# Optimization experiments

Measured on AMD Instinct MI355X. Metric: run time of the kernel, lower is better.

The kernel has to match this reference:

```python
import jax, jax.numpy as jnp
import numpy as np

V_IN, V_OUT = 128, 128
E_IN, E_OUT = 64, 64
H, L, D = 256, 2, 2
DEC_H = D * L * H  # 1024
S_IN, B, S_OUT = 128, 512, 64


def _lstm_step(h, c, x, W_ih, W_hh, b):
    # PyTorch gate order: i, f, g, o
    gates = x @ W_ih.T + h @ W_hh.T + b
    i, f, g, o = jnp.split(gates, 4, axis=-1)
    c = jax.nn.sigmoid(f) * c + jax.nn.sigmoid(i) * jnp.tanh(g)
    h = jax.nn.sigmoid(o) * jnp.tanh(c)
    return h, c


def _run_lstm_dir(x_seq, W_ih, W_hh, b, reverse):
    # x_seq: [S, B, in]; returns hidden sequence [S, B, H], final (h, c)
    Bsz = x_seq.shape[1]
    Hd = W_hh.shape[1]
    init = (jnp.zeros((Bsz, Hd), x_seq.dtype), jnp.zeros((Bsz, Hd), x_seq.dtype))

    def step(carry, x):
        h, c = _lstm_step(carry[0], carry[1], x, W_ih, W_hh, b)
        return (h, c), h

    (hf, cf), hs = jax.lax.scan(step, init, x_seq, reverse=reverse)
    return hs, hf, cf


def setup_inputs() -> dict:
    key = jax.random.key(0)
    ks = jax.random.split(key, 20)
    s = 0.05
    inp = {}
    inp["input_tokens"] = jax.random.randint(ks[0], (S_IN, B), 0, V_IN, dtype=jnp.int32)
    inp["output_tokens"] = jax.random.randint(ks[1], (B, S_OUT), 0, V_OUT, dtype=jnp.int32)
    inp["in_emb"] = jax.random.normal(ks[2], (V_IN, E_IN), jnp.float32) * s
    # encoder layer 0: input E_IN; layer 1: input D*H. Leading dim 2 = directions.
    inp["enc_W_ih0"] = jax.random.normal(ks[3], (2, 4 * H, E_IN), jnp.float32) * s
    inp["enc_W_hh0"] = jax.random.normal(ks[4], (2, 4 * H, H), jnp.float32) * s
    inp["enc_b0"] = jax.random.normal(ks[5], (2, 4 * H), jnp.float32) * s
    inp["enc_W_ih1"] = jax.random.normal(ks[6], (2, 4 * H, D * H), jnp.float32) * s
    inp["enc_W_hh1"] = jax.random.normal(ks[7], (2, 4 * H, H), jnp.float32) * s
    inp["enc_b1"] = jax.random.normal(ks[8], (2, 4 * H), jnp.float32) * s
    inp["out_emb"] = jax.random.normal(ks[9], (V_OUT, E_OUT), jnp.float32) * s
    inp["dec_W_ih"] = jax.random.normal(ks[10], (4 * DEC_H, E_OUT), jnp.float32) * s
    inp["dec_W_hh"] = jax.random.normal(ks[11], (4 * DEC_H, DEC_H), jnp.float32) * s
    inp["dec_b"] = jax.random.normal(ks[12], (4 * DEC_H,), jnp.float32) * s
    inp["proj_W"] = jax.random.normal(ks[13], (V_OUT, DEC_H), jnp.float32) * s
    inp["proj_b"] = jax.random.normal(ks[14], (V_OUT,), jnp.float32) * s
    return inp


def reference(input_tokens, output_tokens, in_emb,
              enc_W_ih0, enc_W_hh0, enc_b0,
              enc_W_ih1, enc_W_hh1, enc_b1,
              out_emb, dec_W_ih, dec_W_hh, dec_b, proj_W, proj_b):
    # ---- encoder: 2-layer bidirectional LSTM over [S_in, B] ----
    x = in_emb[input_tokens]  # [S, B, E_IN]
    h_list, c_list = [], []
    for W_ih, W_hh, b in ((enc_W_ih0, enc_W_hh0, enc_b0),
                          (enc_W_ih1, enc_W_hh1, enc_b1)):
        hs_f, hf, cf = _run_lstm_dir(x, W_ih[0], W_hh[0], b[0], False)
        hs_b, hb, cb = _run_lstm_dir(x, W_ih[1], W_hh[1], b[1], True)
        x = jnp.concatenate([hs_f, hs_b], axis=-1)  # [S, B, 2H]
        h_list += [hf, hb]
        c_list += [cf, cb]
    Bsz = x.shape[1]
    # PyTorch h_n order: (l0_fwd, l0_bwd, l1_fwd, l1_bwd) -> swapaxes+reshape
    h0 = jnp.stack(h_list, axis=1).reshape(Bsz, -1)  # [B, D*L*H]
    c0 = jnp.stack(c_list, axis=1).reshape(Bsz, -1)

    # ---- decoder: teacher-forced LSTMCell loop ----
    tok_in = output_tokens[:, :-1].T   # [T-1, B]
    tok_next = output_tokens[:, 1:].T  # [T-1, B]

    def step(carry, toks):
        h, c = carry
        t_in, t_next = toks
        e = out_emb[t_in]                                 # [B, E_OUT]
        h, c = _lstm_step(h, c, e, dec_W_ih, dec_W_hh, dec_b)
        logits = c @ proj_W.T + proj_b                    # NOTE: proj on CELL, as in source
        greedy = jnp.argmax(logits, axis=1)
        lp = jax.nn.log_softmax(logits, axis=-1)
        logp = jnp.take_along_axis(lp, t_next[:, None], axis=1)[:, 0]
        return (h, c), (greedy, logp)

    _, (decoded_tokens, log_probs) = jax.lax.scan(step, (h0, c0), (tok_in, tok_next))
    cum_log_probs = jnp.sum(log_probs, axis=0)  # [B]
    return decoded_tokens, cum_log_probs
```

## Files before the change

kernel.cpp:

```cpp
#include <hip/hip_runtime.h>
#include <math.h>

#define B 512
#define S_IN 128
#define S_OUT 64
#define T_DEC 63

#define O_H0   0
#define O_H1   (512*1024)
#define O_C    (2*512*1024)
#define O_CUM  (3*512*1024)
#define O_HS0  (O_CUM + 512)
#define O_P1   (O_HS0 + 128*512*512)

template<int MODE>
__global__ __launch_bounds__(256)
void enc_step(const float* __restrict__ Wih, const float* __restrict__ Whh,
              const float* __restrict__ bias, const int* __restrict__ tok,
              const float* __restrict__ emb, const float* __restrict__ seqin,
              const float* __restrict__ h_in, float* __restrict__ h_out,
              float* __restrict__ c_st, float* __restrict__ seqout,
              const float* __restrict__ p1, int t)
{
    constexpr int KE = (MODE==0) ? 64 : (MODE==2 ? 512 : 0);
    constexpr int K  = KE + 256;
    constexpr int NK = K/16;

    const int dir   = blockIdx.z;
    const int t_eff = dir ? (S_IN-1-t) : t;
    const int hseg  = (MODE==0) ? dir*256 : 512 + dir*256;

    const float* Wih_d = Wih + (size_t)dir*1024*KE;
    const float* Whh_d = Whh + (size_t)dir*1024*256;
    const float* b_d   = bias + dir*1024;

    __shared__ float As[16][64];
    __shared__ float Bs[16][64];

    const int tid = threadIdx.x;
    const int bm0 = blockIdx.x*64;
    const int bn0 = blockIdx.y*64;

    const int la_m  = tid >> 2;
    const int la_k  = (tid & 3) << 2;
    const int a_row = bm0 + la_m;

    const int lb_n = tid >> 2;
    const int lb_k = (tid & 3) << 2;
    const int n_g  = bn0 + lb_n;
    const int b_j  = (n_g & 3)*256 + (n_g >> 2);

    int tokidx = 0;
    if (MODE==0) tokidx = tok[t_eff*B + a_row];

    const int tm = (tid >> 4) << 2;
    const int tn = (tid & 15) << 2;

    float acc[4][4] = {};

    auto loadA = [&](int kt) -> float4 {
        int k = kt*16 + la_k;
        if (MODE==0) {
            if (k < 64) return *(const float4*)&emb[(size_t)tokidx*64 + k];
            return *(const float4*)&h_in[(size_t)a_row*1024 + hseg + (k-64)];
        } else if (MODE==2) {
            if (k < 512) return *(const float4*)&seqin[((size_t)t_eff*B + a_row)*512 + k];
            return *(const float4*)&h_in[(size_t)a_row*1024 + hseg + (k-512)];
        } else {
            return *(const float4*)&h_in[(size_t)a_row*1024 + hseg + k];
        }
    };
    auto loadB = [&](int kt) -> float4 {
        int k = kt*16 + lb_k;
        if (KE && k < KE) return *(const float4*)&Wih_d[(size_t)b_j*KE + k];
        return *(const float4*)&Whh_d[(size_t)b_j*256 + (k-KE)];
    };

    float4 aR = loadA(0), bR = loadB(0);
    for (int kt=0; kt<NK; ++kt) {
        __syncthreads();
        As[la_k+0][la_m]=aR.x; As[la_k+1][la_m]=aR.y; As[la_k+2][la_m]=aR.z; As[la_k+3][la_m]=aR.w;
        Bs[lb_k+0][lb_n]=bR.x; Bs[lb_k+1][lb_n]=bR.y; Bs[lb_k+2][lb_n]=bR.z; Bs[lb_k+3][lb_n]=bR.w;
        __syncthreads();
        if (kt+1 < NK) { aR = loadA(kt+1); bR = loadB(kt+1); }
        #pragma unroll
        for (int k=0;k<16;k++){
            const float4 a = *(const float4*)&As[k][tm];
            const float4 b = *(const float4*)&Bs[k][tn];
            acc[0][0]+=a.x*b.x; acc[0][1]+=a.x*b.y; acc[0][2]+=a.x*b.z; acc[0][3]+=a.x*b.w;
            acc[1][0]+=a.y*b.x; acc[1][1]+=a.y*b.y; acc[1][2]+=a.y*b.z; acc[1][3]+=a.y*b.w;
            acc[2][0]+=a.z*b.x; acc[2][1]+=a.z*b.y; acc[2][2]+=a.z*b.z; acc[2][3]+=a.z*b.w;
            acc[3][0]+=a.w*b.x; acc[3][1]+=a.w*b.y; acc[3][2]+=a.w*b.z; acc[3][3]+=a.w*b.w;
        }
    }

    const int jh = (bn0 + tn) >> 2;
    const float bi = b_d[0*256 + jh];
    const float bf = b_d[1*256 + jh];
    const float bg = b_d[2*256 + jh];
    const float bo = b_d[3*256 + jh];
    #pragma unroll
    for (int i=0;i<4;i++){
        const int brow = bm0 + tm + i;
        float xi = acc[i][0] + bi;
        float xf = acc[i][1] + bf;
        float xg = acc[i][2] + bg;
        float xo = acc[i][3] + bo;
        if (MODE==1) {
            const float4 pv = *(const float4*)&p1[((size_t)dir*512 + brow)*1024 + bn0 + tn];
            xi += pv.x; xf += pv.y; xg += pv.z; xo += pv.w;
        }
        float ig = 1.f/(1.f+expf(-xi));
        float fg = 1.f/(1.f+expf(-xf));
        float gg = tanhf(xg);
        float og = 1.f/(1.f+expf(-xo));
        size_t ci = (size_t)brow*1024 + hseg + jh;
        float cn = fg*c_st[ci] + ig*gg;
        float hn = og*tanhf(cn);
        c_st[ci]  = cn;
        h_out[ci] = hn;
        if (MODE==0) seqout[((size_t)t_eff*B + brow)*512 + dir*256 + jh] = hn;
    }
}

template<int MODE>
__global__ __launch_bounds__(128)
void gemm128(const float* __restrict__ Wih, const float* __restrict__ Whh,
             const float* __restrict__ bias, const int* __restrict__ tok,
             const float* __restrict__ emb, const float* __restrict__ hs0,
             const float* __restrict__ h_in, float* __restrict__ h_out,
             float* __restrict__ c_st, float* __restrict__ p1out, int t_or_s0)
{
    constexpr int KE = (MODE==0) ? 64 : 0;
    constexpr int K  = (MODE==0) ? 1088 : 512;
    constexpr int NK = K/16;
    constexpr int HH = (MODE==0) ? 1024 : 256;

    const int dir = (MODE==1) ? blockIdx.z : 0;

    __shared__ float As[16][64];
    __shared__ float Bs[16][64];

    const int tid = threadIdx.x;
    const int bm0 = blockIdx.x*64;
    const int bn0 = blockIdx.y*64;

    const int la_m  = tid >> 1;
    const int la_k  = (tid & 1) << 3;
    const int a_row = bm0 + la_m;

    const int srel  = (MODE==1) ? (blockIdx.x >> 3) : 0;
    const int sabs  = (MODE==1) ? (t_or_s0 + srel) : 0;
    const int t_eff = (MODE==1) ? (dir ? (S_IN-1-sabs) : sabs) : 0;
    const int a_b   = a_row & 511;

    const int n_g = bn0 + la_m;
    const int b_j = (n_g & 3)*HH + (n_g >> 2);

    const float* Wih_d = (MODE==1) ? (Wih + (size_t)dir*1024*512) : Wih;

    int tokidx = 0;
    if (MODE==0) tokidx = tok[a_row*S_OUT + t_or_s0];

    const int tm = (tid >> 3) << 2;
    const int tn = (tid & 7) << 3;

    float acc[4][8] = {};

    auto loadA = [&](int kt, int q) -> float4 {
        int k = kt*16 + la_k + q*4;
        if (MODE==0) {
            if (k < 64) return *(const float4*)&emb[(size_t)tokidx*64 + k];
            return *(const float4*)&h_in[(size_t)a_row*1024 + (k-64)];
        }
        return *(const float4*)&hs0[((size_t)t_eff*B + a_b)*512 + k];
    };
    auto loadB = [&](int kt, int q) -> float4 {
        int k = kt*16 + la_k + q*4;
        if (MODE==0) {
            if (k < 64) return *(const float4*)&Wih[(size_t)b_j*64 + k];
            return *(const float4*)&Whh[(size_t)b_j*1024 + (k-64)];
        }
        return *(const float4*)&Wih_d[(size_t)b_j*512 + k];
    };

    float4 aR0 = loadA(0,0), aR1 = loadA(0,1);
    float4 bR0 = loadB(0,0), bR1 = loadB(0,1);
    for (int kt=0; kt<NK; ++kt) {
        __syncthreads();
        As[la_k+0][la_m]=aR0.x; As[la_k+1][la_m]=aR0.y; As[la_k+2][la_m]=aR0.z; As[la_k+3][la_m]=aR0.w;
        As[la_k+4][la_m]=aR1.x; As[la_k+5][la_m]=aR1.y; As[la_k+6][la_m]=aR1.z; As[la_k+7][la_m]=aR1.w;
        Bs[la_k+0][la_m]=bR0.x; Bs[la_k+1][la_m]=bR0.y; Bs[la_k+2][la_m]=bR0.z; Bs[la_k+3][la_m]=bR0.w;
        Bs[la_k+4][la_m]=bR1.x; Bs[la_k+5][la_m]=bR1.y; Bs[la_k+6][la_m]=bR1.z; Bs[la_k+7][la_m]=bR1.w;
        __syncthreads();
        if (kt+1 < NK) {
            aR0 = loadA(kt+1,0); aR1 = loadA(kt+1,1);
            bR0 = loadB(kt+1,0); bR1 = loadB(kt+1,1);
        }
        #pragma unroll
        for (int k=0;k<16;k++){
            const float4 a  = *(const float4*)&As[k][tm];
            const float4 b0 = *(const float4*)&Bs[k][tn];
            const float4 b1 = *(const float4*)&Bs[k][tn+4];
            acc[0][0]+=a.x*b0.x; acc[0][1]+=a.x*b0.y; acc[0][2]+=a.x*b0.z; acc[0][3]+=a.x*b0.w;
            acc[0][4]+=a.x*b1.x; acc[0][5]+=a.x*b1.y; acc[0][6]+=a.x*b1.z; acc[0][7]+=a.x*b1.w;
            acc[1][0]+=a.y*b0.x; acc[1][1]+=a.y*b0.y; acc[1][2]+=a.y*b0.z; acc[1][3]+=a.y*b0.w;
            acc[1][4]+=a.y*b1.x; acc[1][5]+=a.y*b1.y; acc[1][6]+=a.y*b1.z; acc[1][7]+=a.y*b1.w;
            acc[2][0]+=a.z*b0.x; acc[2][1]+=a.z*b0.y; acc[2][2]+=a.z*b0.z; acc[2][3]+=a.z*b0.w;
            acc[2][4]+=a.z*b1.x; acc[2][5]+=a.z*b1.y; acc[2][6]+=a.z*b1.z; acc[2][7]+=a.z*b1.w;
            acc[3][0]+=a.w*b0.x; acc[3][1]+=a.w*b0.y; acc[3][2]+=a.w*b0.z; acc[3][3]+=a.w*b0.w;
            acc[3][4]+=a.w*b1.x; acc[3][5]+=a.w*b1.y; acc[3][6]+=a.w*b1.z; acc[3][7]+=a.w*b1.w;
        }
    }

    if (MODE==0) {
        const int jh0 = (bn0 + tn) >> 2;
        #pragma unroll
        for (int u=0;u<2;u++){
            const int jh = jh0 + u;
            const float bi = bias[0*1024 + jh];
            const float bf = bias[1*1024 + jh];
            const float bg = bias[2*1024 + jh];
            const float bo = bias[3*1024 + jh];
            #pragma unroll
            for (int i=0;i<4;i++){
                const int brow = bm0 + tm + i;
                float xi = acc[i][4*u+0] + bi;
                float xf = acc[i][4*u+1] + bf;
                float xg = acc[i][4*u+2] + bg;
                float xo = acc[i][4*u+3] + bo;
                float ig = 1.f/(1.f+expf(-xi));
                float fg = 1.f/(1.f+expf(-xf));
                float gg = tanhf(xg);
                float og = 1.f/(1.f+expf(-xo));
                size_t ci = (size_t)brow*1024 + jh;
                float cn = fg*c_st[ci] + ig*gg;
                float hn = og*tanhf(cn);
                c_st[ci]  = cn;
                h_out[ci] = hn;
            }
        }
    } else {
        #pragma unroll
        for (int i=0;i<4;i++){
            const int r = bm0 + tm + i;
            size_t base = ((size_t)(srel*2 + dir)*512 + (r & 511))*1024 + bn0 + tn;
            *(float4*)&p1out[base]   = *(float4*)&acc[i][0];
            *(float4*)&p1out[base+4] = *(float4*)&acc[i][4];
        }
    }
}

__global__ __launch_bounds__(256)
void proj2(const float* __restrict__ c, const float* __restrict__ pW,
           const float* __restrict__ pb, const int* __restrict__ out_tok,
           float* __restrict__ cum, float* __restrict__ dout, int t)
{
    __shared__ float cs[8][1024];
    __shared__ float ls[8][128];
    const int tid = threadIdx.x;
    const int b0 = blockIdx.x*8;
    #pragma unroll
    for (int r=0;r<8;r++)
        *(float4*)&cs[r][tid*4] = *(const float4*)&c[(size_t)(b0+r)*1024 + tid*4];
    __syncthreads();

    const int wave = tid >> 6, lane = tid & 63;
    const int col  = wave*32 + (lane & 31);
    const int rb   = (lane >> 5) * 4;
    float a0=0.f,a1=0.f,a2=0.f,a3=0.f;
    for (int k=0;k<1024;k+=4){
        const float4 w = *(const float4*)&pW[(size_t)col*1024 + k];
        const float4 c0 = *(const float4*)&cs[rb+0][k];
        const float4 c1 = *(const float4*)&cs[rb+1][k];
        const float4 c2 = *(const float4*)&cs[rb+2][k];
        const float4 c3 = *(const float4*)&cs[rb+3][k];
        a0 += w.x*c0.x + w.y*c0.y + w.z*c0.z + w.w*c0.w;
        a1 += w.x*c1.x + w.y*c1.y + w.z*c1.z + w.w*c1.w;
        a2 += w.x*c2.x + w.y*c2.y + w.z*c2.z + w.w*c2.w;
        a3 += w.x*c3.x + w.y*c3.y + w.z*c3.z + w.w*c3.w;
    }
    const float bb = pb[col];
    ls[rb+0][col]=a0+bb; ls[rb+1][col]=a1+bb; ls[rb+2][col]=a2+bb; ls[rb+3][col]=a3+bb;
    __syncthreads();

    #pragma unroll
    for (int rr=0;rr<2;rr++){
        const int r = wave*2 + rr, b = b0 + r;
        float v0 = ls[r][lane], v1 = ls[r][lane+64];
        float mv; int mi;
        if (v1 > v0) { mv = v1; mi = lane+64; } else { mv = v0; mi = lane; }
        #pragma unroll
        for (int o=32;o>=1;o>>=1){
            float ov = __shfl_xor(mv, o);
            int   oi = __shfl_xor(mi, o);
            if (ov > mv || (ov == mv && oi < mi)) { mv = ov; mi = oi; }
        }
        float e = expf(v0 - mv) + expf(v1 - mv);
        #pragma unroll
        for (int o=32;o>=1;o>>=1) e += __shfl_xor(e, o);
        if (lane == 0){
            const int tnx = out_tok[b*S_OUT + t + 1];
            const float lv = ls[r][tnx];
            const float logp = lv - mv - logf(e);
            const float cn = ((t==0) ? 0.f : cum[b]) + logp;
            cum[b] = cn;
            dout[T_DEC*B + b] = cn;
            dout[t*B + b] = (float)mi;
        }
    }
}

__global__ void zero_kernel(float* __restrict__ p, int n4){
    int i = blockIdx.x*blockDim.x + threadIdx.x;
    if (i < n4) *(float4*)&p[i*4] = float4{0.f,0.f,0.f,0.f};
}

extern "C" void kernel_launch(void* const* d_in, const int* in_sizes, int n_in,
                              void* d_out, int out_size, void* d_ws, size_t ws_size,
                              hipStream_t stream)
{
    const int*   input_tokens  = (const int*)d_in[0];
    const int*   output_tokens = (const int*)d_in[1];
    const float* in_emb  = (const float*)d_in[2];
    const float* eWih0   = (const float*)d_in[3];
    const float* eWhh0   = (const float*)d_in[4];
    const float* eb0     = (const float*)d_in[5];
    const float* eWih1   = (const float*)d_in[6];
    const float* eWhh1   = (const float*)d_in[7];
    const float* eb1     = (const float*)d_in[8];
    const float* out_emb = (const float*)d_in[9];
    const float* dWih    = (const float*)d_in[10];
    const float* dWhh    = (const float*)d_in[11];
    const float* db      = (const float*)d_in[12];
    const float* pW      = (const float*)d_in[13];
    const float* pb      = (const float*)d_in[14];

    size_t ws_fl = ws_size / 4;
    if (ws_fl < (size_t)O_P1) return;

    int CH = 0;
    if      (ws_fl >= (size_t)O_P1 + 16u*1048576u) CH = 16;
    else if (ws_fl >= (size_t)O_P1 +  8u*1048576u) CH = 8;
    else if (ws_fl >= (size_t)O_P1 +  4u*1048576u) CH = 4;
    else if (ws_fl >= (size_t)O_P1 +  2u*1048576u) CH = 2;

    float* ws  = (float*)d_ws;
    float* out = (float*)d_out;

    float* h[2] = { ws + O_H0, ws + O_H1 };
    float* c    = ws + O_C;
    float* cum  = ws + O_CUM;
    float* hs0  = ws + O_HS0;
    float* p1   = ws + O_P1;

    zero_kernel<<<(O_HS0/4 + 255)/256, 256, 0, stream>>>(ws, O_HS0/4);

    for (int t=0;t<S_IN;t++)
        enc_step<0><<<dim3(8,16,2),256,0,stream>>>(eWih0, eWhh0, eb0,
            input_tokens, in_emb, nullptr, h[t&1], h[(t+1)&1], c, hs0, nullptr, t);

    if (CH) {
        for (int s0=0; s0<S_IN; s0+=CH) {
            gemm128<1><<<dim3(CH*8,16,2),128,0,stream>>>(eWih1, nullptr, nullptr,
                nullptr, nullptr, hs0, nullptr, nullptr, nullptr, p1, s0);
            for (int s=s0; s<s0+CH; ++s)
                enc_step<1><<<dim3(8,16,2),256,0,stream>>>(eWih1, eWhh1, eb1,
                    nullptr, nullptr, nullptr, h[s&1], h[(s+1)&1], c, nullptr,
                    p1 + (size_t)(s-s0)*2*512*1024, s);
        }
    } else {
        for (int t=0;t<S_IN;t++)
            enc_step<2><<<dim3(8,16,2),256,0,stream>>>(eWih1, eWhh1, eb1,
                nullptr, nullptr, hs0, h[t&1], h[(t+1)&1], c, nullptr, nullptr, t);
    }

    for (int t=0;t<T_DEC;t++){
        gemm128<0><<<dim3(8,64,1),128,0,stream>>>(dWih, dWhh, db,
            output_tokens, out_emb, nullptr, h[t&1], h[(t+1)&1], c, nullptr, t);
        proj2<<<64,256,0,stream>>>(c, pW, pb, output_tokens, cum, out, t);
    }
}
```

Before: 16.89 ms.

## Fuse decoder loop into a single persistent kernel with grid barriers

Replaces the 63 per-step decoder launches (gate GEMM plus separate projection/softmax kernel) with one persistent 512-block kernel that loops over time steps. A software grid barrier built on an atomic counter separates the gate update from the projection, and the projection from the next step. This removes about 126 kernel launches and their gaps. In exchange, all 512 blocks must be resident at once to avoid deadlock, and the projection now handles one batch row per block, re-reading proj_W from global memory for every row.

```diff
diff --git a/kernel.cpp b/kernel.cpp
--- a/kernel.cpp
+++ b/kernel.cpp
@@ -7,11 +7,11 @@
 #define T_DEC 63
 
 #define O_H0   0
-#define O_H1   (512*1024)
-#define O_C    (2*512*1024)
-#define O_CUM  (3*512*1024)
-#define O_HS0  (O_CUM + 512)
-#define O_P1   (O_HS0 + 128*512*512)
+#define O_H1   524288
+#define O_C    1048576
+#define O_BAR  1572864
+#define O_HS0  1572868
+#define O_P1   (O_HS0 + 33554432)
 
 template<int MODE>
 __global__ __launch_bounds__(256)
@@ -123,20 +123,12 @@
     }
 }
 
-template<int MODE>
 __global__ __launch_bounds__(128)
-void gemm128(const float* __restrict__ Wih, const float* __restrict__ Whh,
-             const float* __restrict__ bias, const int* __restrict__ tok,
-             const float* __restrict__ emb, const float* __restrict__ hs0,
-             const float* __restrict__ h_in, float* __restrict__ h_out,
-             float* __restrict__ c_st, float* __restrict__ p1out, int t_or_s0)
+void gemm_p1(const float* __restrict__ Wih, const float* __restrict__ hs0,
+             float* __restrict__ p1out, int s0)
 {
-    constexpr int KE = (MODE==0) ? 64 : 0;
-    constexpr int K  = (MODE==0) ? 1088 : 512;
-    constexpr int NK = K/16;
-    constexpr int HH = (MODE==0) ? 1024 : 256;
-
-    const int dir = (MODE==1) ? blockIdx.z : 0;
+    constexpr int NK = 512/16;
+    const int dir = blockIdx.z;
 
     __shared__ float As[16][64];
     __shared__ float Bs[16][64];
@@ -149,18 +141,15 @@
     const int la_k  = (tid & 1) << 3;
     const int a_row = bm0 + la_m;
 
-    const int srel  = (MODE==1) ? (blockIdx.x >> 3) : 0;
-    const int sabs  = (MODE==1) ? (t_or_s0 + srel) : 0;
-    const int t_eff = (MODE==1) ? (dir ? (S_IN-1-sabs) : sabs) : 0;
+    const int srel  = blockIdx.x >> 3;
+    const int sabs  = s0 + srel;
+    const int t_eff = dir ? (S_IN-1-sabs) : sabs;
     const int a_b   = a_row & 511;
 
     const int n_g = bn0 + la_m;
-    const int b_j = (n_g & 3)*HH + (n_g >> 2);
-
-    const float* Wih_d = (MODE==1) ? (Wih + (size_t)dir*1024*512) : Wih;
-
-    int tokidx = 0;
-    if (MODE==0) tokidx = tok[a_row*S_OUT + t_or_s0];
+    const int b_j = (n_g & 3)*256 + (n_g >> 2);
+
+    const float* Wih_d = Wih + (size_t)dir*1024*512;
 
     const int tm = (tid >> 3) << 2;
     const int tn = (tid & 7) << 3;
@@ -169,18 +158,10 @@
 
     auto loadA = [&](int kt, int q) -> float4 {
         int k = kt*16 + la_k + q*4;
-        if (MODE==0) {
-            if (k < 64) return *(const float4*)&emb[(size_t)tokidx*64 + k];
-            return *(const float4*)&h_in[(size_t)a_row*1024 + (k-64)];
-        }
         return *(const float4*)&hs0[((size_t)t_eff*B + a_b)*512 + k];
     };
     auto loadB = [&](int kt, int q) -> float4 {
         int k = kt*16 + la_k + q*4;
-        if (MODE==0) {
-            if (k < 64) return *(const float4*)&Wih[(size_t)b_j*64 + k];
-            return *(const float4*)&Whh[(size_t)b_j*1024 + (k-64)];
-        }
         return *(const float4*)&Wih_d[(size_t)b_j*512 + k];
     };
 
@@ -213,8 +194,101 @@
         }
     }
 
-    if (MODE==0) {
-        const int jh0 = (bn0 + tn) >> 2;
+    #pragma unroll
+    for (int i=0;i<4;i++){
+        const int r = bm0 + tm + i;
+        size_t base = ((size_t)(srel*2 + dir)*512 + (r & 511))*1024 + bn0 + tn;
+        *(float4*)&p1out[base]   = *(float4*)&acc[i][0];
+        *(float4*)&p1out[base+4] = *(float4*)&acc[i][4];
+    }
+}
+
+__device__ __forceinline__ void grid_bar(unsigned* cnt, unsigned target)
+{
+    __syncthreads();
+    if (threadIdx.x == 0) {
+        __threadfence();
+        atomicAdd(cnt, 1u);
+        while (__hip_atomic_load(cnt, __ATOMIC_ACQUIRE, __HIP_MEMORY_SCOPE_AGENT) < target) {
+            __builtin_amdgcn_s_sleep(2);
+        }
+        __threadfence();
+    }
+    __syncthreads();
+}
+
+__global__ __launch_bounds__(128)
+void dec_persist(const float* __restrict__ Wih, const float* __restrict__ Whh,
+                 const float* __restrict__ bias, const int* __restrict__ tok,
+                 const float* __restrict__ emb, const float* __restrict__ pW,
+                 const float* __restrict__ pb, float* __restrict__ h0b,
+                 float* __restrict__ h1b, float* __restrict__ c_st,
+                 unsigned* __restrict__ bar, float* __restrict__ dout)
+{
+    __shared__ float As[16][64];
+    __shared__ float Bs[16][64];
+    __shared__ float cs[1024];
+    __shared__ float ls[128];
+
+    const int b   = blockIdx.x, tid = threadIdx.x;
+    const int bm0 = (b & 7) << 6;
+    const int bn0 = (b >> 3) << 6;
+
+    const int la_m  = tid >> 1;
+    const int la_k  = (tid & 1) << 3;
+    const int a_row = bm0 + la_m;
+    const int n_g   = bn0 + la_m;
+    const int b_j   = (n_g & 3)*1024 + (n_g >> 2);
+    const int tm    = (tid >> 3) << 2;
+    const int tn    = (tid & 7) << 3;
+    const int jh0   = (bn0 + tn) >> 2;
+
+    for (int t = 0; t < T_DEC; ++t) {
+        const float* h_in  = (t & 1) ? h1b : h0b;
+        float*       h_out = (t & 1) ? h0b : h1b;
+        const int tokidx = tok[a_row*S_OUT + t];
+
+        float acc[4][8] = {};
+        auto loadA = [&](int kt, int q) -> float4 {
+            int k = kt*16 + la_k + q*4;
+            if (k < 64) return *(const float4*)&emb[(size_t)tokidx*64 + k];
+            return *(const float4*)&h_in[(size_t)a_row*1024 + (k-64)];
+        };
+        auto loadB = [&](int kt, int q) -> float4 {
+            int k = kt*16 + la_k + q*4;
+            if (k < 64) return *(const float4*)&Wih[(size_t)b_j*64 + k];
+            return *(const float4*)&Whh[(size_t)b_j*1024 + (k-64)];
+        };
+
+        float4 aR0 = loadA(0,0), aR1 = loadA(0,1);
+        float4 bR0 = loadB(0,0), bR1 = loadB(0,1);
+        for (int kt=0; kt<68; ++kt) {
+            __syncthreads();
+            As[la_k+0][la_m]=aR0.x; As[la_k+1][la_m]=aR0.y; As[la_k+2][la_m]=aR0.z; As[la_k+3][la_m]=aR0.w;
+            As[la_k+4][la_m]=aR1.x; As[la_k+5][la_m]=aR1.y; As[la_k+6][la_m]=aR1.z; As[la_k+7][la_m]=aR1.w;
+            Bs[la_k+0][la_m]=bR0.x; Bs[la_k+1][la_m]=bR0.y; Bs[la_k+2][la_m]=bR0.z; Bs[la_k+3][la_m]=bR0.w;
+            Bs[la_k+4][la_m]=bR1.x; Bs[la_k+5][la_m]=bR1.y; Bs[la_k+6][la_m]=bR1.z; Bs[la_k+7][la_m]=bR1.w;
+            __syncthreads();
+            if (kt+1 < 68) {
+                aR0 = loadA(kt+1,0); aR1 = loadA(kt+1,1);
+                bR0 = loadB(kt+1,0); bR1 = loadB(kt+1,1);
+            }
+            #pragma unroll
+            for (int k=0;k<16;k++){
+                const float4 a  = *(const float4*)&As[k][tm];
+                const float4 b0 = *(const float4*)&Bs[k][tn];
+                const float4 b1 = *(const float4*)&Bs[k][tn+4];
+                acc[0][0]+=a.x*b0.x; acc[0][1]+=a.x*b0.y; acc[0][2]+=a.x*b0.z; acc[0][3]+=a.x*b0.w;
+                acc[0][4]+=a.x*b1.x; acc[0][5]+=a.x*b1.y; acc[0][6]+=a.x*b1.z; acc[0][7]+=a.x*b1.w;
+                acc[1][0]+=a.y*b0.x; acc[1][1]+=a.y*b0.y; acc[1][2]+=a.y*b0.z; acc[1][3]+=a.y*b0.w;
+                acc[1][4]+=a.y*b1.x; acc[1][5]+=a.y*b1.y; acc[1][6]+=a.y*b1.z; acc[1][7]+=a.y*b1.w;
+                acc[2][0]+=a.z*b0.x; acc[2][1]+=a.z*b0.y; acc[2][2]+=a.z*b0.z; acc[2][3]+=a.z*b0.w;
+                acc[2][4]+=a.z*b1.x; acc[2][5]+=a.z*b1.y; acc[2][6]+=a.z*b1.z; acc[2][7]+=a.z*b1.w;
+                acc[3][0]+=a.w*b0.x; acc[3][1]+=a.w*b0.y; acc[3][2]+=a.w*b0.z; acc[3][3]+=a.w*b0.w;
+                acc[3][4]+=a.w*b1.x; acc[3][5]+=a.w*b1.y; acc[3][6]+=a.w*b1.z; acc[3][7]+=a.w*b1.w;
+            }
+        }
+
         #pragma unroll
         for (int u=0;u<2;u++){
             const int jh = jh0 + u;
@@ -240,74 +314,47 @@
                 h_out[ci] = hn;
             }
         }
-    } else {
+
+        grid_bar(bar, (unsigned)(2*t+1) * 512u);
+
         #pragma unroll
-        for (int i=0;i<4;i++){
-            const int r = bm0 + tm + i;
-            size_t base = ((size_t)(srel*2 + dir)*512 + (r & 511))*1024 + bn0 + tn;
-            *(float4*)&p1out[base]   = *(float4*)&acc[i][0];
-            *(float4*)&p1out[base+4] = *(float4*)&acc[i][4];
-        }
-    }
-}
-
-__global__ __launch_bounds__(256)
-void proj2(const float* __restrict__ c, const float* __restrict__ pW,
-           const float* __restrict__ pb, const int* __restrict__ out_tok,
-           float* __restrict__ cum, float* __restrict__ dout, int t)
-{
-    __shared__ float cs[8][1024];
-    __shared__ float ls[8][128];
-    const int tid = threadIdx.x;
-    const int b0 = blockIdx.x*8;
-    #pragma unroll
-    for (int r=0;r<8;r++)
-        *(float4*)&cs[r][tid*4] = *(const float4*)&c[(size_t)(b0+r)*1024 + tid*4];
-    __syncthreads();
-
-    const int wave = tid >> 6, lane = tid & 63;
-    const int col  = wave*32 + (lane & 31);
-    const int rb   = (lane >> 5) * 4;
-    float a0=0.f,a1=0.f,a2=0.f,a3=0.f;
-    for (int k=0;k<1024;k+=4){
-        const float4 w = *(const float4*)&pW[(size_t)col*1024 + k];
-        const float4 c0 = *(const float4*)&cs[rb+0][k];
-        const float4 c1 = *(const float4*)&cs[rb+1][k];
-        const float4 c2 = *(const float4*)&cs[rb+2][k];
-        const float4 c3 = *(const float4*)&cs[rb+3][k];
-        a0 += w.x*c0.x + w.y*c0.y + w.z*c0.z + w.w*c0.w;
-        a1 += w.x*c1.x + w.y*c1.y + w.z*c1.z + w.w*c1.w;
-        a2 += w.x*c2.x + w.y*c2.y + w.z*c2.z + w.w*c2.w;
-        a3 += w.x*c3.x + w.y*c3.y + w.z*c3.z + w.w*c3.w;
-    }
-    const float bb = pb[col];
-    ls[rb+0][col]=a0+bb; ls[rb+1][col]=a1+bb; ls[rb+2][col]=a2+bb; ls[rb+3][col]=a3+bb;
-    __syncthreads();
-
-    #pragma unroll
-    for (int rr=0;rr<2;rr++){
-        const int r = wave*2 + rr, b = b0 + r;
-        float v0 = ls[r][lane], v1 = ls[r][lane+64];
-        float mv; int mi;
-        if (v1 > v0) { mv = v1; mi = lane+64; } else { mv = v0; mi = lane; }
-        #pragma unroll
-        for (int o=32;o>=1;o>>=1){
-            float ov = __shfl_xor(mv, o);
-            int   oi = __shfl_xor(mi, o);
-            if (ov > mv || (ov == mv && oi < mi)) { mv = ov; mi = oi; }
-        }
-        float e = expf(v0 - mv) + expf(v1 - mv);
-        #pragma unroll
-        for (int o=32;o>=1;o>>=1) e += __shfl_xor(e, o);
-        if (lane == 0){
-            const int tnx = out_tok[b*S_OUT + t + 1];
-            const float lv = ls[r][tnx];
-            const float logp = lv - mv - logf(e);
-            const float cn = ((t==0) ? 0.f : cum[b]) + logp;
-            cum[b] = cn;
-            dout[T_DEC*B + b] = cn;
-            dout[t*B + b] = (float)mi;
-        }
+        for (int q=0;q<2;q++)
+            *(float4*)&cs[(q*128+tid)*4] = *(const float4*)&c_st[(size_t)b*1024 + (q*128+tid)*4];
+        __syncthreads();
+        {
+            float a0 = 0.f;
+            for (int k=0;k<1024;k+=4){
+                const float4 w  = *(const float4*)&pW[(size_t)tid*1024 + k];
+                const float4 c0 = *(const float4*)&cs[k];
+                a0 += w.x*c0.x + w.y*c0.y + w.z*c0.z + w.w*c0.w;
+            }
+            ls[tid] = a0 + pb[tid];
+        }
+        __syncthreads();
+        if (tid < 64) {
+            const int lane = tid;
+            const float v0 = ls[lane], v1 = ls[lane+64];
+            float mv; int mi;
+            if (v1 > v0){ mv=v1; mi=lane+64; } else { mv=v0; mi=lane; }
+            #pragma unroll
+            for (int o=32;o>=1;o>>=1){
+                const float ov = __shfl_xor(mv, o);
+                const int   oi = __shfl_xor(mi, o);
+                if (ov > mv || (ov == mv && oi < mi)){ mv=ov; mi=oi; }
+            }
+            float e = expf(v0-mv) + expf(v1-mv);
+            #pragma unroll
+            for (int o=32;o>=1;o>>=1) e += __shfl_xor(e, o);
+            if (lane == 0){
+                const int tnx = tok[b*S_OUT + t + 1];
+                const float logp = ls[tnx] - mv - logf(e);
+                const float cn = ((t==0)?0.f:dout[T_DEC*B + b]) + logp;
+                dout[T_DEC*B + b] = cn;
+                dout[t*B + b] = (float)mi;
+            }
+        }
+
+        grid_bar(bar, (unsigned)(2*t+2) * 512u);
     }
 }
 
@@ -345,14 +392,14 @@
     else if (ws_fl >= (size_t)O_P1 +  4u*1048576u) CH = 4;
     else if (ws_fl >= (size_t)O_P1 +  2u*1048576u) CH = 2;
 
-    float* ws  = (float*)d_ws;
-    float* out = (float*)d_out;
-
-    float* h[2] = { ws + O_H0, ws + O_H1 };
-    float* c    = ws + O_C;
-    float* cum  = ws + O_CUM;
-    float* hs0  = ws + O_HS0;
-    float* p1   = ws + O_P1;
+    float* ws   = (float*)d_ws;
+    float* dout = (float*)d_out;
+
+    float* h[2]   = { ws + O_H0, ws + O_H1 };
+    float* c      = ws + O_C;
+    unsigned* bar = (unsigned*)(ws + O_BAR);
+    float* hs0    = ws + O_HS0;
+    float* p1     = ws + O_P1;
 
     zero_kernel<<<(O_HS0/4 + 255)/256, 256, 0, stream>>>(ws, O_HS0/4);
 
@@ -362,8 +409,7 @@
 
     if (CH) {
         for (int s0=0; s0<S_IN; s0+=CH) {
-            gemm128<1><<<dim3(CH*8,16,2),128,0,stream>>>(eWih1, nullptr, nullptr,
-                nullptr, nullptr, hs0, nullptr, nullptr, nullptr, p1, s0);
+            gemm_p1<<<dim3(CH*8,16,2),128,0,stream>>>(eWih1, hs0, p1, s0);
             for (int s=s0; s<s0+CH; ++s)
                 enc_step<1><<<dim3(8,16,2),256,0,stream>>>(eWih1, eWhh1, eb1,
                     nullptr, nullptr, nullptr, h[s&1], h[(s+1)&1], c, nullptr,
@@ -375,9 +421,6 @@
                 nullptr, nullptr, hs0, h[t&1], h[(t+1)&1], c, nullptr, nullptr, t);
     }
 
-    for (int t=0;t<T_DEC;t++){
-        gemm128<0><<<dim3(8,64,1),128,0,stream>>>(dWih, dWhh, db,
-            output_tokens, out_emb, nullptr, h[t&1], h[(t+1)&1], c, nullptr, t);
-        proj2<<<64,256,0,stream>>>(c, pW, pb, output_tokens, cum, out, t);
-    }
-}
+    dec_persist<<<512,128,0,stream>>>(dWih, dWhh, db, output_tokens, out_emb,
+                                      pW, pb, h[0], h[1], c, bar, dout);
+}
```

Measured after the change: 24.47 ms. 1.45x slower.
